# Optimization experiments

Hardware: AMD Instinct MI355X
Metric: run time of the kernel (lower is better)

The kernel has to match this reference:

```python
import jax, jax.numpy as jnp
import numpy as np

N_QUBITS = 12
RANK = 1024
K = 4            # outcomes per qubit
D = 2 ** N_QUBITS
N_IDX = 1_000_000


def setup_inputs() -> dict:
    key = jax.random.key(0)
    k1, k2, k3, k4 = jax.random.split(key, 4)
    params = jax.random.normal(k1, (2, D, RANK), dtype=jnp.float32)
    M_real = jax.random.normal(k2, (K, 2, 2), dtype=jnp.float32)
    M_imag = jax.random.normal(k3, (K, 2, 2), dtype=jnp.float32)
    P_idxs = jax.random.randint(k4, (N_IDX,), 0, K ** N_QUBITS, dtype=jnp.int64)
    return {"params": params, "M_real": M_real, "M_imag": M_imag, "P_idxs": P_idxs}


def _qmt(rho, M, n_qubits):
    """Born rule: P[s1..sN] = Tr[(M_{s1} x ... x M_{sN}) rho].
    Sequential per-qubit contraction; T has shape [K^n, 2^(N-n), 2^(N-n)]."""
    T = rho[None, :, :]  # axes: (done outcomes, row legs j, col legs i)
    for _ in range(n_qubits):
        k, r, c = T.shape[0], T.shape[1] // 2, T.shape[2] // 2
        Tt = T.reshape(k, 2, r, 2, c)  # (k, j_n, j_rest, i_n, i_rest)
        # Tr contribution: sum_{i,j} M[s,i,j] * rho[j,i]
        T = jnp.einsum('sij,kjait->ksat', M, Tt).reshape(k * M.shape[0], r, c)
    return T.reshape(-1)  # [K^N] complex


def reference(params, M_real, M_imag, P_idxs):
    # rho = U U^H / Tr(U U^H)
    U = jax.lax.complex(params[0], params[1])            # [D, RANK] complex64
    rho = U @ U.conj().T                                  # [D, D]
    rho = rho / jnp.trace(rho)
    M = jax.lax.complex(M_real, M_imag)                   # [K, 2, 2] complex64
    P_all = _qmt(rho, M, N_QUBITS).real                   # [K^N] float32
    return P_all[P_idxs]
```

## Files before the change

### kernel.cpp

```cpp
#include <hip/hip_runtime.h>

#define D 4096
#define RANK 1024
#define UELEMS 4194304ULL
#define NTOT 16777216ULL
#define QSCALE 16000.0f

typedef __attribute__((ext_vector_type(4))) int i32x4;

__device__ float g_inv_tr[1];
__device__ float g_scale[D];
__device__ float g_mdre[16];
__device__ float g_mdim[16];

static __device__ __forceinline__ void load_lds16(const void* g, void* l) {
    __builtin_amdgcn_global_load_lds(
        (const __attribute__((address_space(1))) unsigned int*)g,
        (__attribute__((address_space(3))) unsigned int*)l, 16, 0, 0);
}

#define MFMA_I8 __builtin_amdgcn_mfma_i32_16x16x64_i8

__global__ __launch_bounds__(256) void convert_w_i8(const float* __restrict__ P,
                                                    const float* __restrict__ Mre,
                                                    const float* __restrict__ Mim,
                                                    char* __restrict__ Wh,
                                                    char* __restrict__ Wl)
{
    if (blockIdx.x == 0 && threadIdx.x < 16) {
        const int s = threadIdx.x >> 2, i = (threadIdx.x >> 1) & 1, j = threadIdx.x & 1;
        g_mdre[threadIdx.x] =  Mre[s * 4 + j * 2 + i];
        g_mdim[threadIdx.x] = -Mim[s * 4 + j * 2 + i];
    }

    const int w = threadIdx.x >> 6, lane = threadIdx.x & 63;
    const int row = blockIdx.x * 4 + w;

    float ur[16], ui[16];
    const float* pr = P + (size_t)row * RANK + lane * 16;
    const float* pi = P + UELEMS + (size_t)row * RANK + lane * 16;
    #pragma unroll
    for (int q = 0; q < 4; ++q) {
        const float4 a = ((const float4*)pr)[q];
        const float4 b = ((const float4*)pi)[q];
        ur[q * 4 + 0] = a.x; ur[q * 4 + 1] = a.y; ur[q * 4 + 2] = a.z; ur[q * 4 + 3] = a.w;
        ui[q * 4 + 0] = b.x; ui[q * 4 + 1] = b.y; ui[q * 4 + 2] = b.z; ui[q * 4 + 3] = b.w;
    }
    float mx = 0.f;
    #pragma unroll
    for (int e = 0; e < 16; ++e)
        mx = fmaxf(mx, fmaxf(fabsf(ur[e]), fabsf(ui[e])));
    #pragma unroll
    for (int off = 1; off < 64; off <<= 1)
        mx = fmaxf(mx, __shfl_xor(mx, off));
    const float inv = mx > 0.f ? QSCALE / mx : 0.f;
    if (lane == 0) g_scale[row] = mx / QSCALE;

    int hr[16], lr[16], hi[16], li[16];
    #pragma unroll
    for (int e = 0; e < 16; ++e) {
        float q = ur[e] * inv;
        float hf = rintf(q * 0.0078125f);
        hr[e] = (int)hf; lr[e] = (int)rintf(q - 128.f * hf);
        q = ui[e] * inv;
        hf = rintf(q * 0.0078125f);
        hi[e] = (int)hf; li[e] = (int)rintf(q - 128.f * hf);
    }
    uint4 phr, plr, phi, pli;
    unsigned* dst[4] = {(unsigned*)&phr, (unsigned*)&plr, (unsigned*)&phi, (unsigned*)&pli};
    #pragma unroll
    for (int q = 0; q < 4; ++q) {
        unsigned a = 0, b = 0, c = 0, d = 0;
        #pragma unroll
        for (int k = 0; k < 4; ++k) {
            const int sh = k * 8;
            a |= (unsigned)(hr[q * 4 + k] & 255) << sh;
            b |= (unsigned)(lr[q * 4 + k] & 255) << sh;
            c |= (unsigned)(hi[q * 4 + k] & 255) << sh;
            d |= (unsigned)(li[q * 4 + k] & 255) << sh;
        }
        dst[0][q] = a; dst[1][q] = b; dst[2][q] = c; dst[3][q] = d;
    }
    const size_t b1 = (size_t)row * 2048 + lane * 16;
    *(uint4*)&Wh[b1] = phr;          *(uint4*)&Wl[b1] = plr;
    *(uint4*)&Wh[b1 + 1024] = phi;   *(uint4*)&Wl[b1 + 1024] = pli;
}

__global__ __launch_bounds__(256, 2) void gemm_rho_i8(const char* __restrict__ Wh,
                                                      const char* __restrict__ Wl,
                                                      float2* __restrict__ rho)
{
    __shared__ __align__(16) char sA[2][4][64 * 64];
    __shared__ __align__(16) char sB[2][4][64 * 64];

    const int g0 = blockIdx.x;
    const int g = (g0 & 7) * 260 + (g0 >> 3);

    int bi = (int)((sqrtf(8.f * (float)g + 1.f) - 1.f) * 0.5f);
    while (bi * (bi + 1) / 2 > g) --bi;
    while ((bi + 1) * (bi + 2) / 2 <= g) ++bi;
    const int bj = g - bi * (bi + 1) / 2;
    const int row0 = bi << 6, col0 = bj << 6;

    const int t = threadIdx.x;
    const int lane = t & 63, w = t >> 6;
    const int wr = w >> 1, wc = w & 1;

    const int ra = t >> 2;
    const int kca = (t & 3) ^ ((ra >> 1) & 3);
    const size_t aoff = (size_t)(row0 + ra) * 2048 + kca * 16;
    const size_t boff = (size_t)(col0 + ra) * 2048 + kca * 16;
    const int ldso = t * 16;

    const int m = lane & 15, gq = lane >> 4;
    const int fko = (gq ^ ((m >> 1) & 3)) * 16;

    i32x4 rehh[2][2], remx[2][2], iphh[2][2], ipmx[2][2], iqhh[2][2], iqmx[2][2];
    #pragma unroll
    for (int i = 0; i < 2; ++i)
        #pragma unroll
        for (int j = 0; j < 2; ++j) {
            rehh[i][j] = (i32x4){0, 0, 0, 0}; remx[i][j] = (i32x4){0, 0, 0, 0};
            iphh[i][j] = (i32x4){0, 0, 0, 0}; ipmx[i][j] = (i32x4){0, 0, 0, 0};
            iqhh[i][j] = (i32x4){0, 0, 0, 0}; iqmx[i][j] = (i32x4){0, 0, 0, 0};
        }

    char* const sA0 = &sA[0][0][0];
    char* const sB0 = &sB[0][0][0];

    load_lds16(Wh + aoff,        sA0 + ldso);
    load_lds16(Wl + aoff,        sA0 + 4096  + ldso);
    load_lds16(Wh + aoff + 1024, sA0 + 8192  + ldso);
    load_lds16(Wl + aoff + 1024, sA0 + 12288 + ldso);
    load_lds16(Wh + boff,        sB0 + ldso);
    load_lds16(Wl + boff,        sB0 + 4096  + ldso);
    load_lds16(Wh + boff + 1024, sB0 + 8192  + ldso);
    load_lds16(Wl + boff + 1024, sB0 + 12288 + ldso);
    __syncthreads();

#define DO_MFMA_J(j)                                                          \
    _Pragma("unroll")                                                         \
    for (int i = 0; i < 2; ++i) {                                             \
        i32x4 r;                                                              \
        r = rehh[i][j];                                                       \
        r = MFMA_I8(fa1h[i], b1h[j], r, 0, 0, 0);                             \
        r = MFMA_I8(fa2h[i], b2h[j], r, 0, 0, 0);                             \
        rehh[i][j] = r;                                                       \
        r = remx[i][j];                                                       \
        r = MFMA_I8(fa1h[i], b1l[j], r, 0, 0, 0);                             \
        r = MFMA_I8(fa1l[i], b1h[j], r, 0, 0, 0);                             \
        r = MFMA_I8(fa2h[i], b2l[j], r, 0, 0, 0);                             \
        r = MFMA_I8(fa2l[i], b2h[j], r, 0, 0, 0);                             \
        remx[i][j] = r;                                                       \
        r = MFMA_I8(fa2h[i], b1h[j], iphh[i][j], 0, 0, 0); iphh[i][j] = r;    \
        r = ipmx[i][j];                                                       \
        r = MFMA_I8(fa2h[i], b1l[j], r, 0, 0, 0);                             \
        r = MFMA_I8(fa2l[i], b1h[j], r, 0, 0, 0);                             \
        ipmx[i][j] = r;                                                       \
        r = MFMA_I8(fa1h[i], b2h[j], iqhh[i][j], 0, 0, 0); iqhh[i][j] = r;    \
        r = iqmx[i][j];                                                       \
        r = MFMA_I8(fa1h[i], b2l[j], r, 0, 0, 0);                             \
        r = MFMA_I8(fa1l[i], b2h[j], r, 0, 0, 0);                             \
        iqmx[i][j] = r;                                                       \
    }

    #pragma unroll 2
    for (int kt = 0; kt < 16; ++kt) {
        const int cur = kt & 1;
        const char* sAc = sA0 + cur * 16384;
        const char* sBc = sB0 + cur * 16384;
        char* sAn = sA0 + (cur ^ 1) * 16384;
        char* sBn = sB0 + (cur ^ 1) * 16384;
        const size_t ko = (size_t)(kt + 1) * 64;

        if (kt < 15) {
            load_lds16(Wh + aoff + ko,        sAn + ldso);
            load_lds16(Wl + aoff + ko,        sAn + 4096  + ldso);
            load_lds16(Wh + aoff + ko + 1024, sAn + 8192  + ldso);
            load_lds16(Wl + aoff + ko + 1024, sAn + 12288 + ldso);
            load_lds16(Wh + boff + ko,        sBn + ldso);
            load_lds16(Wl + boff + ko,        sBn + 4096  + ldso);
            load_lds16(Wh + boff + ko + 1024, sBn + 8192  + ldso);
            load_lds16(Wl + boff + ko + 1024, sBn + 12288 + ldso);
        }

        i32x4 fa1h[2], fa1l[2], fa2h[2], fa2l[2];
        i32x4 b1h[2], b1l[2], b2h[2], b2l[2];
        #pragma unroll
        for (int i = 0; i < 2; ++i) {
            const int off = (wr * 32 + i * 16 + m) * 64 + fko;
            fa1h[i] = *(const i32x4*)(sAc + off);
            fa1l[i] = *(const i32x4*)(sAc + 4096  + off);
            fa2h[i] = *(const i32x4*)(sAc + 8192  + off);
            fa2l[i] = *(const i32x4*)(sAc + 12288 + off);
        }
        #pragma unroll
        for (int j = 0; j < 2; ++j) {
            const int off = (wc * 32 + j * 16 + m) * 64 + fko;
            b1h[j] = *(const i32x4*)(sBc + off);
            b1l[j] = *(const i32x4*)(sBc + 4096  + off);
            b2h[j] = *(const i32x4*)(sBc + 8192  + off);
            b2l[j] = *(const i32x4*)(sBc + 12288 + off);
        }

        __builtin_amdgcn_s_setprio(1);
        DO_MFMA_J(0)
        DO_MFMA_J(1)
        __builtin_amdgcn_s_setprio(0);

        __syncthreads();
    }
#undef DO_MFMA_J

    #pragma unroll
    for (int j = 0; j < 2; ++j) {
        const int col = col0 + wc * 32 + j * 16 + m;
        const float sc = g_scale[col];
        const int c64 = col >> 6;
        #pragma unroll
        for (int i = 0; i < 2; ++i) {
            #pragma unroll
            for (int r = 0; r < 4; ++r) {
                const int row = row0 + wr * 32 + i * 16 + gq * 4 + r;
                const float s2 = g_scale[row] * sc;
                const float re = s2 * (16384.f * (float)rehh[i][j][r] + 128.f * (float)remx[i][j][r]);
                const float im = s2 * (16384.f * (float)(iphh[i][j][r] - iqhh[i][j][r])
                                      + 128.f * (float)(ipmx[i][j][r] - iqmx[i][j][r]));
                const int r64 = row >> 6;
                if (r64 > c64 || row >= col) rho[(size_t)row * D + col] = make_float2(re, im);
                if (r64 == c64 && row > col) rho[(size_t)col * D + row] = make_float2(re, -im);
            }
        }
    }
}

__global__ void trace_inv(const float2* __restrict__ rho)
{
    __shared__ float red[256];
    float s = 0.f;
    for (int d = threadIdx.x; d < D; d += 256)
        s += rho[(size_t)d * (D + 1)].x;
    red[threadIdx.x] = s;
    __syncthreads();
    for (int off = 128; off > 0; off >>= 1) {
        if (threadIdx.x < off) red[threadIdx.x] += red[threadIdx.x + off];
        __syncthreads();
    }
    if (threadIdx.x == 0) g_inv_tr[0] = 1.0f / red[0];
}

static __device__ __forceinline__ void qmt2(float2* x,
                                            const float* __restrict__ Mre,
                                            const float* __restrict__ Mim)
{
    float2 y[16];
    #pragma unroll
    for (int sb = 0; sb < 4; ++sb)
        #pragma unroll
        for (int ja = 0; ja < 2; ++ja)
            #pragma unroll
            for (int ia = 0; ia < 2; ++ia) {
                float2 acc = make_float2(0.f, 0.f);
                #pragma unroll
                for (int ib = 0; ib < 2; ++ib)
                    #pragma unroll
                    for (int jb = 0; jb < 2; ++jb) {
                        const float mr = Mre[sb * 4 + ib * 2 + jb];
                        const float mi = Mim[sb * 4 + ib * 2 + jb];
                        const float2 v = x[(ja * 2 + jb) * 4 + ia * 2 + ib];
                        acc.x += mr * v.x - mi * v.y;
                        acc.y += mr * v.y + mi * v.x;
                    }
                y[sb * 4 + ja * 2 + ia] = acc;
            }
    #pragma unroll
    for (int sa = 0; sa < 4; ++sa)
        #pragma unroll
        for (int sb = 0; sb < 4; ++sb) {
            float2 acc = make_float2(0.f, 0.f);
            #pragma unroll
            for (int ia = 0; ia < 2; ++ia)
                #pragma unroll
                for (int ja = 0; ja < 2; ++ja) {
                    const float mr = Mre[sa * 4 + ia * 2 + ja];
                    const float mi = Mim[sa * 4 + ia * 2 + ja];
                    const float2 v = y[sb * 4 + ja * 2 + ia];
                    acc.x += mr * v.x - mi * v.y;
                    acc.y += mr * v.y + mi * v.x;
                }
            x[sa * 4 + sb] = acc;
        }
}

static __device__ __forceinline__ void pA_pipeline(float2* x, float2* X, const int t,
                                                   const float* __restrict__ mre,
                                                   const float* __restrict__ mim)
{
    qmt2(x, mre, mim);
    #pragma unroll
    for (int d = 0; d < 16; ++d) X[t * 17 + d] = x[d];
    __syncthreads();
    const int a2 = t >> 6, t2 = (t >> 4) & 3, d1 = t & 15;
    #pragma unroll
    for (int j2 = 0; j2 < 4; ++j2)
        #pragma unroll
        for (int i2 = 0; i2 < 4; ++i2)
            x[j2 * 4 + i2] = X[((a2 * 4 + j2) * 16 + t2 * 4 + i2) * 17 + d1];
    __syncthreads();
    qmt2(x, mre, mim);
    #pragma unroll
    for (int d = 0; d < 16; ++d) X[(a2 * 4 + t2) * 257 + d * 16 + d1] = x[d];
    __syncthreads();
    const int e2 = t >> 4, e1 = t & 15;
    #pragma unroll
    for (int j2 = 0; j2 < 4; ++j2)
        #pragma unroll
        for (int i2 = 0; i2 < 4; ++i2)
            x[j2 * 4 + i2] = X[(j2 * 4 + i2) * 257 + e2 * 16 + e1];
    qmt2(x, mre, mim);
}

__global__ __launch_bounds__(256) void qmt_pAh(const float2* __restrict__ in,
                                               float2* __restrict__ out,
                                               const float* __restrict__ Mre,
                                               const float* __restrict__ Mim)
{
    __shared__ __align__(16) float2 X[256 * 17];
    const int t = threadIdx.x;
    const int g = blockIdx.x;
    int rr = (int)((sqrtf(8.f * (float)g + 1.f) - 1.f) * 0.5f);
    while (rr * (rr + 1) / 2 > g) --rr;
    while ((rr + 1) * (rr + 2) / 2 <= g) ++rr;
    const int cc = g - rr * (rr + 1) / 2;

    const int a4 = t >> 4, t4 = t & 15;
    float2 x0[16], x[16];
    #pragma unroll
    for (int j2 = 0; j2 < 4; ++j2) {
        const float2* p = in + ((size_t)(rr * 64 + a4 * 4 + j2)) * 4096 + cc * 64 + t4 * 4;
        const float4 v0 = ((const float4*)p)[0];
        const float4 v1 = ((const float4*)p)[1];
        x0[j2 * 4 + 0] = make_float2(v0.x, v0.y);
        x0[j2 * 4 + 1] = make_float2(v0.z, v0.w);
        x0[j2 * 4 + 2] = make_float2(v1.x, v1.y);
        x0[j2 * 4 + 3] = make_float2(v1.z, v1.w);
    }

    #pragma unroll
    for (int q = 0; q < 16; ++q) x[q] = x0[q];
    pA_pipeline(x, X, t, Mre, Mim);
    const int e2 = t >> 4, e1 = t & 15;
    const size_t ob0 = (size_t)(rr * 64 + cc) * 4096 + e2 * 16 + e1;
    #pragma unroll
    for (int d = 0; d < 16; ++d) out[ob0 + (size_t)d * 256] = x[d];

    if (rr != cc) {
        __syncthreads();
        #pragma unroll
        for (int q = 0; q < 16; ++q) x[q] = x0[q];
        pA_pipeline(x, X, t, g_mdre, g_mdim);
        const size_t ob1 = (size_t)(cc * 64 + rr) * 4096 + e2 * 16 + e1;
        #pragma unroll
        for (int d = 0; d < 16; ++d)
            out[ob1 + (size_t)d * 256] = make_float2(x[d].x, -x[d].y);
    }
}

static __device__ __forceinline__ void qmt_stage_cb_half(float2* x,
                                                         const float* __restrict__ Mre,
                                                         const float* __restrict__ Mim)
{
    #pragma unroll
    for (int jb = 0; jb < 2; ++jb) {
        float2 y[16];
        #pragma unroll
        for (int sc = 0; sc < 4; ++sc)
            #pragma unroll
            for (int ii = 0; ii < 4; ++ii) {
                float2 acc = make_float2(0.f, 0.f);
                #pragma unroll
                for (int ic = 0; ic < 2; ++ic)
                    #pragma unroll
                    for (int jc = 0; jc < 2; ++jc) {
                        const float mr = Mre[sc * 4 + ic * 2 + jc];
                        const float mi = Mim[sc * 4 + ic * 2 + jc];
                        const float2 v = x[jb * 16 + jc * 8 + ii * 2 + ic];
                        acc.x += mr * v.x - mi * v.y;
                        acc.y += mr * v.y + mi * v.x;
                    }
                y[sc * 4 + ii] = acc;
            }
        #pragma unroll
        for (int q = 0; q < 16; ++q) x[jb * 16 + q] = y[q];
    }
    #pragma unroll
    for (int sc = 0; sc < 4; ++sc) {
        float2 z[8];
        #pragma unroll
        for (int sb = 0; sb < 4; ++sb)
            #pragma unroll
            for (int ia = 0; ia < 2; ++ia) {
                float2 acc = make_float2(0.f, 0.f);
                #pragma unroll
                for (int ib = 0; ib < 2; ++ib)
                    #pragma unroll
                    for (int jb = 0; jb < 2; ++jb) {
                        const float mr = Mre[sb * 4 + ib * 2 + jb];
                        const float mi = Mim[sb * 4 + ib * 2 + jb];
                        const float2 v = x[jb * 16 + sc * 4 + ia * 2 + ib];
                        acc.x += mr * v.x - mi * v.y;
                        acc.y += mr * v.y + mi * v.x;
                    }
                z[sb * 2 + ia] = acc;
            }
        #pragma unroll
        for (int sb = 0; sb < 4; ++sb)
            #pragma unroll
            for (int ia = 0; ia < 2; ++ia)
                x[(sb >> 1) * 16 + sc * 4 + ia * 2 + (sb & 1)] = z[sb * 2 + ia];
    }
}

#define STAGE_A_COEFFS                                                        \
    float Are[2][2], Aim[2][2], Bre[2][2], Bim[2][2];                         \
    _Pragma("unroll")                                                         \
    for (int sal = 0; sal < 2; ++sal)                                         \
        _Pragma("unroll")                                                     \
        for (int ia = 0; ia < 2; ++ia) {                                      \
            const int sa = 2 * h + sal;                                       \
            Are[sal][ia] = Mre[sa * 4 + ia * 2 + h];                          \
            Aim[sal][ia] = Mim[sa * 4 + ia * 2 + h];                          \
            Bre[sal][ia] = Mre[sa * 4 + ia * 2 + (1 - h)];                    \
            Bim[sal][ia] = Mim[sa * 4 + ia * 2 + (1 - h)];                    \
        }

__global__ __launch_bounds__(256) void qmt_p3(const float2* __restrict__ in,
                                              float2* __restrict__ out,
                                              const float* __restrict__ Mre,
                                              const float* __restrict__ Mim)
{
    const int t = threadIdx.x;
    const int h = (t >> 5) & 1;
    const int idx = blockIdx.x * 4 + (t >> 6);
    const int rc = idx >> 7;
    const int r3 = rc >> 3, c3 = rc & 7;
    const int s = (idx & 127) * 32 + (t & 31);

    float2 x[32];
    #pragma unroll
    for (int jb = 0; jb < 2; ++jb)
        #pragma unroll
        for (int jc = 0; jc < 2; ++jc) {
            const int j3 = 4 * h + 2 * jb + jc;
            #pragma unroll
            for (int i3 = 0; i3 < 8; ++i3)
                x[jb * 16 + jc * 8 + i3] =
                    in[(size_t)((r3 * 8 + j3) * 64 + c3 * 8 + i3) * 4096 + s];
        }

    qmt_stage_cb_half(x, Mre, Mim);

    STAGE_A_COEFFS
    const size_t ob = ((size_t)(r3 * 8 + c3) * 64) * 4096 + s;
    #pragma unroll
    for (int sbH = 0; sbH < 2; ++sbH)
        #pragma unroll
        for (int sc = 0; sc < 4; ++sc)
            #pragma unroll
            for (int sbL = 0; sbL < 2; ++sbL) {
                const int q = sbH * 16 + sc * 4 + sbL;
                const float2 o0 = x[q], o1 = x[q + 2];
                float2 r0, r1;
                r0.x = __shfl_xor(o0.x, 32); r0.y = __shfl_xor(o0.y, 32);
                r1.x = __shfl_xor(o1.x, 32); r1.y = __shfl_xor(o1.y, 32);
                const int sb = sbH * 2 + sbL;
                #pragma unroll
                for (int sal = 0; sal < 2; ++sal) {
                    const float re = Are[sal][0] * o0.x - Aim[sal][0] * o0.y
                                   + Are[sal][1] * o1.x - Aim[sal][1] * o1.y
                                   + Bre[sal][0] * r0.x - Bim[sal][0] * r0.y
                                   + Bre[sal][1] * r1.x - Bim[sal][1] * r1.y;
                    const float im = Are[sal][0] * o0.y + Aim[sal][0] * o0.x
                                   + Are[sal][1] * o1.y + Aim[sal][1] * o1.x
                                   + Bre[sal][0] * r0.y + Bim[sal][0] * r0.x
                                   + Bre[sal][1] * r1.y + Bim[sal][1] * r1.x;
                    const int s3 = (2 * h + sal) * 16 + sb * 4 + sc;
                    out[ob + (size_t)s3 * 4096] = make_float2(re, im);
                }
            }
}

__global__ __launch_bounds__(256) void qmt_p4(const float2* __restrict__ in,
                                              float* __restrict__ out,
                                              const float* __restrict__ Mre,
                                              const float* __restrict__ Mim)
{
    const int t = threadIdx.x;
    const int h = (t >> 5) & 1;
    const int s = (blockIdx.x * 4 + (t >> 6)) * 32 + (t & 31);

    float2 x[32];
    #pragma unroll
    for (int jb = 0; jb < 2; ++jb)
        #pragma unroll
        for (int jc = 0; jc < 2; ++jc) {
            const int j3 = 4 * h + 2 * jb + jc;
            #pragma unroll
            for (int i3 = 0; i3 < 8; ++i3)
                x[jb * 16 + jc * 8 + i3] = in[(size_t)(j3 * 8 + i3) * 262144 + s];
        }

    qmt_stage_cb_half(x, Mre, Mim);

    STAGE_A_COEFFS
    const size_t ob = (size_t)(s >> 5) * 2048 + (s & 31);
    #pragma unroll
    for (int sbH = 0; sbH < 2; ++sbH)
        #pragma unroll
        for (int sc = 0; sc < 4; ++sc)
            #pragma unroll
            for (int sbL = 0; sbL < 2; ++sbL) {
                const int q = sbH * 16 + sc * 4 + sbL;
                const float2 o0 = x[q], o1 = x[q + 2];
                float2 r0, r1;
                r0.x = __shfl_xor(o0.x, 32); r0.y = __shfl_xor(o0.y, 32);
                r1.x = __shfl_xor(o1.x, 32); r1.y = __shfl_xor(o1.y, 32);
                const int sb = sbH * 2 + sbL;
                #pragma unroll
                for (int sal = 0; sal < 2; ++sal) {
                    const float re = Are[sal][0] * o0.x - Aim[sal][0] * o0.y
                                   + Are[sal][1] * o1.x - Aim[sal][1] * o1.y
                                   + Bre[sal][0] * r0.x - Bim[sal][0] * r0.y
                                   + Bre[sal][1] * r1.x - Bim[sal][1] * r1.y;
                    const int s3 = (2 * h + sal) * 16 + sb * 4 + sc;
                    out[ob + (size_t)s3 * 32] = re;
                }
            }
}

__global__ void gather_idx(const float* __restrict__ P, const int* __restrict__ idxs,
                           float* __restrict__ out, const int n)
{
    const int i = blockIdx.x * 256 + threadIdx.x;
    if (i < n) {
        const int idx = idxs[i];
        const int s = idx & 262143;
        const size_t pos = (size_t)(s >> 5) * 2048 + (size_t)(idx >> 18) * 32 + (s & 31);
        out[i] = P[pos] * g_inv_tr[0];
    }
}

extern "C" void kernel_launch(void* const* d_in, const int* in_sizes, int n_in,
                              void* d_out, int out_size, void* d_ws, size_t ws_size,
                              hipStream_t stream)
{
    const float* params = (const float*)d_in[0];
    const float* Mre    = (const float*)d_in[1];
    const float* Mim    = (const float*)d_in[2];
    const int*   idxs   = (const int*)d_in[3];
    float*       out    = (float*)d_out;

    float* ws = (float*)d_ws;
    float2* A  = (float2*)ws;
    float2* Bp = (float2*)(ws + 2 * NTOT);
    char* Wh = (char*)Bp;
    char* Wl = Wh + (size_t)D * 2048;

    convert_w_i8<<<1024, 256, 0, stream>>>(params, Mre, Mim, Wh, Wl);
    gemm_rho_i8<<<2080, 256, 0, stream>>>(Wh, Wl, A);
    trace_inv<<<1, 256, 0, stream>>>(A);

    qmt_pAh<<<2080, 256, 0, stream>>>(A, Bp, Mre, Mim);
    qmt_p3<<<2048, 256, 0, stream>>>(Bp, A, Mre, Mim);
    qmt_p4<<<2048, 256, 0, stream>>>(A, (float*)Bp, Mre, Mim);

    gather_idx<<<(out_size + 255) / 256, 256, 0, stream>>>((float*)Bp, idxs, out, out_size);
}
```

Measured before the change: 395.7 us.

## Fuse final two QMT passes into one shared-memory pipeline kernel

Measured after the change: 366.2 us. -7.5%, faster.

```diff
diff --git a/kernel.cpp b/kernel.cpp
--- a/kernel.cpp
+++ b/kernel.cpp
@@ -346,196 +346,58 @@
         x0[j2 * 4 + 3] = make_float2(v1.z, v1.w);
     }
 
+    const size_t wbase = (size_t)(t >> 4) * 65536 + (t & 15);
+
     #pragma unroll
     for (int q = 0; q < 16; ++q) x[q] = x0[q];
     pA_pipeline(x, X, t, Mre, Mim);
-    const int e2 = t >> 4, e1 = t & 15;
-    const size_t ob0 = (size_t)(rr * 64 + cc) * 4096 + e2 * 16 + e1;
-    #pragma unroll
-    for (int d = 0; d < 16; ++d) out[ob0 + (size_t)d * 256] = x[d];
+    {
+        const size_t rc0 = (size_t)(rr * 64 + cc) * 16;
+        #pragma unroll
+        for (int d = 0; d < 16; ++d)
+            out[(size_t)d * 1048576 + wbase + rc0] = x[d];
+    }
 
     if (rr != cc) {
         __syncthreads();
         #pragma unroll
         for (int q = 0; q < 16; ++q) x[q] = x0[q];
         pA_pipeline(x, X, t, g_mdre, g_mdim);
-        const size_t ob1 = (size_t)(cc * 64 + rr) * 4096 + e2 * 16 + e1;
+        const size_t rc1 = (size_t)(cc * 64 + rr) * 16;
         #pragma unroll
         for (int d = 0; d < 16; ++d)
-            out[ob1 + (size_t)d * 256] = make_float2(x[d].x, -x[d].y);
-    }
-}
-
-static __device__ __forceinline__ void qmt_stage_cb_half(float2* x,
-                                                         const float* __restrict__ Mre,
-                                                         const float* __restrict__ Mim)
-{
-    #pragma unroll
-    for (int jb = 0; jb < 2; ++jb) {
-        float2 y[16];
-        #pragma unroll
-        for (int sc = 0; sc < 4; ++sc)
-            #pragma unroll
-            for (int ii = 0; ii < 4; ++ii) {
-                float2 acc = make_float2(0.f, 0.f);
-                #pragma unroll
-                for (int ic = 0; ic < 2; ++ic)
-                    #pragma unroll
-                    for (int jc = 0; jc < 2; ++jc) {
-                        const float mr = Mre[sc * 4 + ic * 2 + jc];
-                        const float mi = Mim[sc * 4 + ic * 2 + jc];
-                        const float2 v = x[jb * 16 + jc * 8 + ii * 2 + ic];
-                        acc.x += mr * v.x - mi * v.y;
-                        acc.y += mr * v.y + mi * v.x;
-                    }
-                y[sc * 4 + ii] = acc;
-            }
-        #pragma unroll
-        for (int q = 0; q < 16; ++q) x[jb * 16 + q] = y[q];
-    }
-    #pragma unroll
-    for (int sc = 0; sc < 4; ++sc) {
-        float2 z[8];
-        #pragma unroll
-        for (int sb = 0; sb < 4; ++sb)
-            #pragma unroll
-            for (int ia = 0; ia < 2; ++ia) {
-                float2 acc = make_float2(0.f, 0.f);
-                #pragma unroll
-                for (int ib = 0; ib < 2; ++ib)
-                    #pragma unroll
-                    for (int jb = 0; jb < 2; ++jb) {
-                        const float mr = Mre[sb * 4 + ib * 2 + jb];
-                        const float mi = Mim[sb * 4 + ib * 2 + jb];
-                        const float2 v = x[jb * 16 + sc * 4 + ia * 2 + ib];
-                        acc.x += mr * v.x - mi * v.y;
-                        acc.y += mr * v.y + mi * v.x;
-                    }
-                z[sb * 2 + ia] = acc;
-            }
-        #pragma unroll
-        for (int sb = 0; sb < 4; ++sb)
-            #pragma unroll
-            for (int ia = 0; ia < 2; ++ia)
-                x[(sb >> 1) * 16 + sc * 4 + ia * 2 + (sb & 1)] = z[sb * 2 + ia];
-    }
-}
-
-#define STAGE_A_COEFFS                                                        \
-    float Are[2][2], Aim[2][2], Bre[2][2], Bim[2][2];                         \
-    _Pragma("unroll")                                                         \
-    for (int sal = 0; sal < 2; ++sal)                                         \
-        _Pragma("unroll")                                                     \
-        for (int ia = 0; ia < 2; ++ia) {                                      \
-            const int sa = 2 * h + sal;                                       \
-            Are[sal][ia] = Mre[sa * 4 + ia * 2 + h];                          \
-            Aim[sal][ia] = Mim[sa * 4 + ia * 2 + h];                          \
-            Bre[sal][ia] = Mre[sa * 4 + ia * 2 + (1 - h)];                    \
-            Bim[sal][ia] = Mim[sa * 4 + ia * 2 + (1 - h)];                    \
-        }
-
-__global__ __launch_bounds__(256) void qmt_p3(const float2* __restrict__ in,
-                                              float2* __restrict__ out,
-                                              const float* __restrict__ Mre,
-                                              const float* __restrict__ Mim)
-{
+            out[(size_t)d * 1048576 + wbase + rc1] = make_float2(x[d].x, -x[d].y);
+    }
+}
+
+__global__ __launch_bounds__(256) void qmt_p34(const float2* __restrict__ in,
+                                               float* __restrict__ out,
+                                               const float* __restrict__ Mre,
+                                               const float* __restrict__ Mim)
+{
+    __shared__ __align__(16) float2 X[256 * 17];
     const int t = threadIdx.x;
-    const int h = (t >> 5) & 1;
-    const int idx = blockIdx.x * 4 + (t >> 6);
-    const int rc = idx >> 7;
-    const int r3 = rc >> 3, c3 = rc & 7;
-    const int s = (idx & 127) * 32 + (t & 31);
-
-    float2 x[32];
-    #pragma unroll
-    for (int jb = 0; jb < 2; ++jb)
-        #pragma unroll
-        for (int jc = 0; jc < 2; ++jc) {
-            const int j3 = 4 * h + 2 * jb + jc;
-            #pragma unroll
-            for (int i3 = 0; i3 < 8; ++i3)
-                x[jb * 16 + jc * 8 + i3] =
-                    in[(size_t)((r3 * 8 + j3) * 64 + c3 * 8 + i3) * 4096 + s];
-        }
-
-    qmt_stage_cb_half(x, Mre, Mim);
-
-    STAGE_A_COEFFS
-    const size_t ob = ((size_t)(r3 * 8 + c3) * 64) * 4096 + s;
-    #pragma unroll
-    for (int sbH = 0; sbH < 2; ++sbH)
-        #pragma unroll
-        for (int sc = 0; sc < 4; ++sc)
-            #pragma unroll
-            for (int sbL = 0; sbL < 2; ++sbL) {
-                const int q = sbH * 16 + sc * 4 + sbL;
-                const float2 o0 = x[q], o1 = x[q + 2];
-                float2 r0, r1;
-                r0.x = __shfl_xor(o0.x, 32); r0.y = __shfl_xor(o0.y, 32);
-                r1.x = __shfl_xor(o1.x, 32); r1.y = __shfl_xor(o1.y, 32);
-                const int sb = sbH * 2 + sbL;
-                #pragma unroll
-                for (int sal = 0; sal < 2; ++sal) {
-                    const float re = Are[sal][0] * o0.x - Aim[sal][0] * o0.y
-                                   + Are[sal][1] * o1.x - Aim[sal][1] * o1.y
-                                   + Bre[sal][0] * r0.x - Bim[sal][0] * r0.y
-                                   + Bre[sal][1] * r1.x - Bim[sal][1] * r1.y;
-                    const float im = Are[sal][0] * o0.y + Aim[sal][0] * o0.x
-                                   + Are[sal][1] * o1.y + Aim[sal][1] * o1.x
-                                   + Bre[sal][0] * r0.y + Bim[sal][0] * r0.x
-                                   + Bre[sal][1] * r1.y + Bim[sal][1] * r1.x;
-                    const int s3 = (2 * h + sal) * 16 + sb * 4 + sc;
-                    out[ob + (size_t)s3 * 4096] = make_float2(re, im);
-                }
-            }
-}
-
-__global__ __launch_bounds__(256) void qmt_p4(const float2* __restrict__ in,
-                                              float* __restrict__ out,
-                                              const float* __restrict__ Mre,
-                                              const float* __restrict__ Mim)
-{
-    const int t = threadIdx.x;
-    const int h = (t >> 5) & 1;
-    const int s = (blockIdx.x * 4 + (t >> 6)) * 32 + (t & 31);
-
-    float2 x[32];
-    #pragma unroll
-    for (int jb = 0; jb < 2; ++jb)
-        #pragma unroll
-        for (int jc = 0; jc < 2; ++jc) {
-            const int j3 = 4 * h + 2 * jb + jc;
-            #pragma unroll
-            for (int i3 = 0; i3 < 8; ++i3)
-                x[jb * 16 + jc * 8 + i3] = in[(size_t)(j3 * 8 + i3) * 262144 + s];
-        }
-
-    qmt_stage_cb_half(x, Mre, Mim);
-
-    STAGE_A_COEFFS
-    const size_t ob = (size_t)(s >> 5) * 2048 + (s & 31);
-    #pragma unroll
-    for (int sbH = 0; sbH < 2; ++sbH)
-        #pragma unroll
-        for (int sc = 0; sc < 4; ++sc)
-            #pragma unroll
-            for (int sbL = 0; sbL < 2; ++sbL) {
-                const int q = sbH * 16 + sc * 4 + sbL;
-                const float2 o0 = x[q], o1 = x[q + 2];
-                float2 r0, r1;
-                r0.x = __shfl_xor(o0.x, 32); r0.y = __shfl_xor(o0.y, 32);
-                r1.x = __shfl_xor(o1.x, 32); r1.y = __shfl_xor(o1.y, 32);
-                const int sb = sbH * 2 + sbL;
-                #pragma unroll
-                for (int sal = 0; sal < 2; ++sal) {
-                    const float re = Are[sal][0] * o0.x - Aim[sal][0] * o0.y
-                                   + Are[sal][1] * o1.x - Aim[sal][1] * o1.y
-                                   + Bre[sal][0] * r0.x - Bim[sal][0] * r0.y
-                                   + Bre[sal][1] * r1.x - Bim[sal][1] * r1.y;
-                    const int s3 = (2 * h + sal) * 16 + sb * 4 + sc;
-                    out[ob + (size_t)s3 * 32] = re;
-                }
-            }
+    const int b = blockIdx.x;
+    const int d34 = (b & 7) * 512 + (b >> 3);
+    const int ohi = d34 >> 4, olo = d34 & 15;
+
+    const float2* base = in + (size_t)ohi * 65536 + olo;
+    const int a4 = t >> 4, t4 = t & 15;
+    float2 x[16];
+    #pragma unroll
+    for (int j2 = 0; j2 < 4; ++j2) {
+        const int rcr = (a4 * 4 + j2) * 64 + t4 * 4;
+        #pragma unroll
+        for (int i2 = 0; i2 < 4; ++i2)
+            x[j2 * 4 + i2] = base[(size_t)(rcr + i2) * 16];
+    }
+
+    pA_pipeline(x, X, t, Mre, Mim);
+
+    const size_t ob = (size_t)d34 * 4096 + t;
+    #pragma unroll
+    for (int d = 0; d < 16; ++d)
+        out[ob + (size_t)d * 256] = x[d].x;
 }
 
 __global__ void gather_idx(const float* __restrict__ P, const int* __restrict__ idxs,
@@ -544,8 +406,7 @@
     const int i = blockIdx.x * 256 + threadIdx.x;
     if (i < n) {
         const int idx = idxs[i];
-        const int s = idx & 262143;
-        const size_t pos = (size_t)(s >> 5) * 2048 + (size_t)(idx >> 18) * 32 + (s & 31);
+        const size_t pos = (size_t)(idx & 4095) * 4096 + (idx >> 12);
         out[i] = P[pos] * g_inv_tr[0];
     }
 }
@@ -571,8 +432,7 @@
     trace_inv<<<1, 256, 0, stream>>>(A);
 
     qmt_pAh<<<2080, 256, 0, stream>>>(A, Bp, Mre, Mim);
-    qmt_p3<<<2048, 256, 0, stream>>>(Bp, A, Mre, Mim);
-    qmt_p4<<<2048, 256, 0, stream>>>(A, (float*)Bp, Mre, Mim);
-
-    gather_idx<<<(out_size + 255) / 256, 256, 0, stream>>>((float*)Bp, idxs, out, out_size);
-}
+    qmt_p34<<<4096, 256, 0, stream>>>(Bp, (float*)A, Mre, Mim);
+
+    gather_idx<<<(out_size + 255) / 256, 256, 0, stream>>>((float*)A, idxs, out, out_size);
+}
```
